# Kernel optimization log

Hardware: AMD Instinct MI355X
Metric: run time of the kernel (lower is better)

The kernel has to match this reference:

```python
import jax, jax.numpy as jnp
import numpy as np

N_NODES = 2048
N_EDGES = 8192
EDGE_DIM = 10
EDGE_HIDDEN = 32
HID = 160


def nnconv(x, edge_index, edge_attr, w1, b1, w2, b2, root, bias):
    """PyG-style NNConv with aggr='mean'.
    x: [N, HID], edge_attr: [E, EDGE_DIM], edge_index: [2, E] (src, dst).
    Per-edge weight W_e = MLP(e) reshaped to [HID, HID]; message = x[src] @ W_e,
    mean-aggregated at dst, plus root transform and bias.
    """
    n = x.shape[0]
    h = jax.nn.relu(edge_attr @ w1 + b1)                     # [E, EDGE_HIDDEN]
    W = (h @ w2 + b2).reshape(-1, HID, HID)                  # [E, HID, HID]
    src, dst = edge_index[0], edge_index[1]
    msg = jnp.einsum('ei,eio->eo', x[src], W)                # [E, HID]
    summed = jax.ops.segment_sum(msg, dst, num_segments=n)   # [N, HID]
    cnt = jax.ops.segment_sum(jnp.ones((msg.shape[0],), x.dtype), dst,
                              num_segments=n)
    aggr = summed / jnp.maximum(cnt, 1.0)[:, None]           # mean; 0 for isolated
    return aggr + x @ root + bias


def setup_inputs() -> dict:
    key = jax.random.key(0)
    ks = jax.random.split(key, 16)
    s = 1.0 / np.sqrt(HID)
    se = 1.0 / np.sqrt(EDGE_DIM)
    sh = 1.0 / np.sqrt(EDGE_HIDDEN)
    inp = {
        'x': jax.random.normal(ks[0], (N_NODES, HID), jnp.float32),
        'edge_attr': jax.random.uniform(ks[1], (N_EDGES, EDGE_DIM), jnp.float32),
        # conv1 (subgraph_conv1) params
        'w1_a': jax.random.normal(ks[2], (EDGE_DIM, EDGE_HIDDEN), jnp.float32) * se,
        'b1_a': jnp.zeros((EDGE_HIDDEN,), jnp.float32),
        'w2_a': jax.random.normal(ks[3], (EDGE_HIDDEN, HID * HID), jnp.float32) * sh,
        'b2_a': jnp.zeros((HID * HID,), jnp.float32),
        'root_a': jax.random.normal(ks[4], (HID, HID), jnp.float32) * s,
        'bias_a': jnp.zeros((HID,), jnp.float32),
        # conv2 (subgraph_conv2, applied twice) params
        'w1_b': jax.random.normal(ks[5], (EDGE_DIM, EDGE_HIDDEN), jnp.float32) * se,
        'b1_b': jnp.zeros((EDGE_HIDDEN,), jnp.float32),
        'w2_b': jax.random.normal(ks[6], (EDGE_HIDDEN, HID * HID), jnp.float32) * sh,
        'b2_b': jnp.zeros((HID * HID,), jnp.float32),
        'root_b': jax.random.normal(ks[7], (HID, HID), jnp.float32) * s,
        'bias_b': jnp.zeros((HID,), jnp.float32),
        'edge_index': jax.random.randint(ks[8], (2, N_EDGES), 0, N_NODES, jnp.int64),
    }
    return inp


def reference(x, edge_attr, w1_a, b1_a, w2_a, b2_a, root_a, bias_a,
              w1_b, b1_b, w2_b, b2_b, root_b, bias_b, edge_index):
    # subgraph_conv1 -> ReLU -> subgraph_conv2 -> ReLU -> subgraph_conv2
    h = jax.nn.relu(nnconv(x, edge_index, edge_attr,
                           w1_a, b1_a, w2_a, b2_a, root_a, bias_a))
    h = jax.nn.relu(nnconv(h, edge_index, edge_attr,
                           w1_b, b1_b, w2_b, b2_b, root_b, bias_b))
    h = nnconv(h, edge_index, edge_attr,
               w1_b, b1_b, w2_b, b2_b, root_b, bias_b)
    return h
```

## Files before the change

kernel.cpp:

```cpp
#include <hip/hip_runtime.h>

#define NN 2048
#define NE 8192
#define ED 10
#define EH 32
#define HID 160
#define NCOL 5504

typedef __attribute__((ext_vector_type(8))) short short8;
typedef __attribute__((ext_vector_type(4))) float f32x4;
typedef unsigned int u32;

__device__ __forceinline__ ushort f2bf(float v) {
    u32 u = __float_as_uint(v);
    u += 0x7FFF + ((u >> 16) & 1);
    return (ushort)(u >> 16);
}
__device__ __forceinline__ float bf2f(ushort u) {
    return __uint_as_float(((u32)u) << 16);
}
__device__ __forceinline__ void gl2lds16(const ushort* g, ushort* l) {
    __builtin_amdgcn_global_load_lds(
        (const __attribute__((address_space(1))) u32*)g,
        (__attribute__((address_space(3))) u32*)l, 16, 0, 0);
}

__global__ __launch_bounds__(256) void k_prep(
        const float* __restrict__ x, ushort* __restrict__ xb,
        const float* __restrict__ ea,
        const float* __restrict__ w1a, const float* __restrict__ b1a,
        const float* __restrict__ w1b, const float* __restrict__ b1b,
        float* __restrict__ ha, float* __restrict__ hb,
        const float* __restrict__ w2a, const float* __restrict__ b2a,
        const float* __restrict__ roota,
        const float* __restrict__ w2b, const float* __restrict__ b2b,
        const float* __restrict__ rootb,
        ushort* __restrict__ BtA, ushort* __restrict__ BtB,
        const int* __restrict__ ei, int* __restrict__ doff,
        int* __restrict__ degg, float* __restrict__ dinv,
        int* __restrict__ delist) {
    __shared__ char smem[20608];
    int b = blockIdx.x, t = threadIdx.x;

    if (b < 512) {
        int set = b >> 8, rel = b & 255;
        const float* w1 = set ? w1b : w1a;
        const float* b1 = set ? b1b : b1a;
        float* h = set ? hb : ha;
        int idx = rel * 1024 + t * 4;
        int e = idx >> 5, j0 = idx & 31;
        float o4[4];
#pragma unroll
        for (int u = 0; u < 4; ++u) {
            float acc = b1[j0 + u];
#pragma unroll
            for (int i = 0; i < ED; ++i) acc += ea[e * ED + i] * w1[i * EH + j0 + u];
            o4[u] = fmaxf(acc, 0.f);
        }
        *(float4*)&h[idx] = *(const float4*)o4;
        return;
    }
    if (b < 856) {
        int rel = b - 512;
        int set = rel / 172, pb = rel - set * 172;
        float (*tile)[161] = (float(*)[161])smem;
        const float* w2 = set ? w2b : w2a;
        const float* b2 = set ? b2b : b2a;
        const float* root = set ? rootb : roota;
        ushort* Bt = set ? BtB : BtA;
        const float* src;
        int n0, zero = 0;
        if (pb < 160)      { int q = pb / 5, op = pb - q * 5; n0 = q * 160 + op * 32; src = w2 + q * 25600 + op * 32; }
        else if (pb < 165) { int ip = pb - 160; n0 = 5120 + ip * 32; src = b2 + ip * 32; }
        else if (pb < 170) { int ip = pb - 165; n0 = 5280 + ip * 32; src = root + ip * 32; }
        else               { n0 = 5440 + (pb - 170) * 32; src = b2; zero = 1; }
        int kl = t >> 5, ol = t & 31;
#pragma unroll
        for (int pass = 0; pass < 20; ++pass) {
            int k = pass * 8 + kl;
            tile[ol][k] = zero ? 0.f : src[k * HID + ol];
        }
        __syncthreads();
        int on = t >> 3, j = t & 7;
        int n = n0 + on;
#pragma unroll
        for (int i = 0; i < 20; i += 2) {
            int k = j * 20 + i;
            u32 pk = ((u32)f2bf(tile[on][k + 1]) << 16) | f2bf(tile[on][k]);
            *(u32*)&Bt[(size_t)n * HID + k] = pk;
        }
        return;
    }
    if (b < 1176) {
        int idx = (b - 856) * 1024 + t * 4;
        float4 xv = *(const float4*)&x[idx];
        ushort o4[4] = {f2bf(xv.x), f2bf(xv.y), f2bf(xv.z), f2bf(xv.w)};
        *(u32*)&xb[idx] = *(const u32*)&o4[0];
        *(u32*)&xb[idx + 2] = *(const u32*)&o4[2];
        return;
    }
    int* deg = (int*)smem;
    int* cur = deg + NN;
    int* part = cur + NN;
    for (int i = t; i < NN; i += 256) deg[i] = 0;
    __syncthreads();
    for (int e = t; e < NE; e += 256) atomicAdd(&deg[ei[NE + e]], 1);
    __syncthreads();
    int loc[8], s = 0;
#pragma unroll
    for (int i = 0; i < 8; ++i) { loc[i] = s; s += deg[t * 8 + i]; }
    part[t] = s;
    __syncthreads();
    int tot = s;
    for (int st = 1; st < 256; st <<= 1) {
        int v = (t >= st) ? part[t - st] : 0;
        __syncthreads();
        part[t] += v;
        __syncthreads();
    }
    int base = part[t] - tot;
#pragma unroll
    for (int i = 0; i < 8; ++i) {
        int d = t * 8 + i;
        doff[d] = base + loc[i];
        cur[d] = base + loc[i];
        degg[d] = deg[d];
        dinv[d] = 1.0f / fmaxf((float)deg[d], 1.0f);
    }
    __syncthreads();
    for (int e = t; e < NE; e += 256) {
        int d = ei[NE + e];
        int p = atomicAdd(&cur[d], 1);
        delist[p] = e;
    }
}

__global__ __launch_bounds__(256) void k_gemm(const ushort* __restrict__ A,
                                              const ushort* __restrict__ B,
                                              ushort* __restrict__ G) {
    __shared__ ushort sA[128 * 32], sB[128 * 32];
    int tid = threadIdx.x;
    int bn = blockIdx.x * 128, bm = blockIdx.y * 128;
    int wid = tid >> 6, lane = tid & 63;
    int wm = (wid >> 1) * 64, wn = (wid & 1) * 64;
    int lr = lane & 15, lk = lane >> 4;
    f32x4 acc[4][4];
#pragma unroll
    for (int i = 0; i < 4; ++i)
#pragma unroll
        for (int j = 0; j < 4; ++j) acc[i][j] = (f32x4){0.f, 0.f, 0.f, 0.f};

    for (int c = 0; c < 5; ++c) {
        int k0 = c * 32;
#pragma unroll
        for (int i = 0; i < 2; ++i) {
            int s = tid + i * 256;
            int r = s >> 2, go = (s & 3) * 8;
            gl2lds16(&A[(size_t)(bm + r) * HID + k0 + go], &sA[s * 8]);
            gl2lds16(&B[(size_t)(bn + r) * HID + k0 + go], &sB[s * 8]);
        }
        __syncthreads();
        short8 av[4];
#pragma unroll
        for (int mt = 0; mt < 4; ++mt)
            av[mt] = *(const short8*)&sA[(wm + mt * 16 + lr) * 32 + lk * 8];
#pragma unroll
        for (int nt = 0; nt < 4; ++nt) {
            short8 bv = *(const short8*)&sB[(wn + nt * 16 + lr) * 32 + lk * 8];
#pragma unroll
            for (int mt = 0; mt < 4; ++mt)
                acc[mt][nt] = __builtin_amdgcn_mfma_f32_16x16x32_bf16(av[mt], bv, acc[mt][nt], 0, 0, 0);
        }
        __syncthreads();
    }
#pragma unroll
    for (int mt = 0; mt < 4; ++mt)
#pragma unroll
        for (int nt = 0; nt < 4; ++nt) {
            int m0 = bm + wm + mt * 16 + lk * 4;
            int n = bn + wn + nt * 16 + lr;
#pragma unroll
            for (int r = 0; r < 4; ++r)
                G[(size_t)(m0 + r) * NCOL + n] = f2bf(acc[mt][nt][r]);
        }
}

__global__ __launch_bounds__(160) void k_aggr(const ushort* __restrict__ G,
        const float* __restrict__ h, const int* __restrict__ ei,
        const int* __restrict__ doff, const int* __restrict__ degg,
        const float* __restrict__ dinv, const int* __restrict__ delist,
        const float* __restrict__ bias, ushort* __restrict__ xn,
        float* __restrict__ out, int last) {
    __shared__ float hbuf[16 * EH];
    __shared__ int ebuf[16], sbuf[16];
    int d = blockIdx.x, t = threadIdx.x;
    int o0 = doff[d], dg = degg[d];
    float acc = 0.f;
    for (int c0 = 0; c0 < dg; c0 += 16) {
        int nc = min(16, dg - c0);
        if (t < nc) {
            int e = delist[o0 + c0 + t];
            ebuf[t] = e;
            sbuf[t] = ei[e];
        }
        __syncthreads();
        for (int i = t; i < nc * EH; i += 160)
            hbuf[i] = h[ebuf[i >> 5] * EH + (i & 31)];
        __syncthreads();
        for (int j = 0; j < nc; ++j) {
            const ushort* Gr = G + (size_t)sbuf[j] * NCOL;
            const float* hj = &hbuf[j * EH];
            float a = bf2f(Gr[5120 + t]);
#pragma unroll
            for (int q = 0; q < 32; ++q)
                a += hj[q] * bf2f(Gr[q * HID + t]);
            acc += a;
        }
        __syncthreads();
    }
    float v = acc * dinv[d] + bf2f(G[(size_t)d * NCOL + 5280 + t]) + bias[t];
    if (last) out[d * HID + t] = v;
    else      xn[d * HID + t] = f2bf(fmaxf(v, 0.f));
}

extern "C" void kernel_launch(void* const* d_in, const int* in_sizes, int n_in,
                              void* d_out, int out_size, void* d_ws, size_t ws_size,
                              hipStream_t stream) {
    const float* x     = (const float*)d_in[0];
    const float* ea    = (const float*)d_in[1];
    const float* w1a   = (const float*)d_in[2];
    const float* b1a   = (const float*)d_in[3];
    const float* w2a   = (const float*)d_in[4];
    const float* b2a   = (const float*)d_in[5];
    const float* roota = (const float*)d_in[6];
    const float* biasa = (const float*)d_in[7];
    const float* w1b   = (const float*)d_in[8];
    const float* b1b   = (const float*)d_in[9];
    const float* w2b   = (const float*)d_in[10];
    const float* b2b   = (const float*)d_in[11];
    const float* rootb = (const float*)d_in[12];
    const float* biasb = (const float*)d_in[13];
    const int*   ei    = (const int*)d_in[14];
    float* out = (float*)d_out;

    char* p = (char*)d_ws;
    ushort* G = (ushort*)p;    p += (size_t)NN * NCOL * 2;
    ushort* BtA = (ushort*)p;  p += (size_t)NCOL * HID * 2;
    ushort* BtB = (ushort*)p;  p += (size_t)NCOL * HID * 2;
    float* h_a = (float*)p;    p += (size_t)NE * EH * 4;
    float* h_b = (float*)p;    p += (size_t)NE * EH * 4;
    ushort* xb0 = (ushort*)p;  p += (size_t)NN * HID * 2;
    ushort* xn = (ushort*)p;   p += (size_t)NN * HID * 2;
    int* doff = (int*)p;       p += NN * 4;
    int* degg = (int*)p;       p += NN * 4;
    float* dinv = (float*)p;   p += NN * 4;
    int* delist = (int*)p;     p += NE * 4;

    k_prep<<<1177, 256, 0, stream>>>(x, xb0, ea, w1a, b1a, w1b, b1b, h_a, h_b,
                                     w2a, b2a, roota, w2b, b2b, rootb, BtA, BtB,
                                     ei, doff, degg, dinv, delist);

    struct Layer { const ushort *xin, *bt; const float *h, *bias; int last; };
    Layer L[3] = {
        {xb0, BtA, h_a, biasa, 0},
        {xn,  BtB, h_b, biasb, 0},
        {xn,  BtB, h_b, biasb, 1},
    };
    for (int l = 0; l < 3; ++l) {
        k_gemm<<<dim3(NCOL / 128, NN / 128), 256, 0, stream>>>(L[l].xin, L[l].bt, G);
        k_aggr<<<NN, 160, 0, stream>>>(G, L[l].h, ei, doff, degg, dinv, delist,
                                       L[l].bias, xn, out, L[l].last);
    }
}
```

Before: 196.8 us.

## Overlap prep work with first GEMM and vectorize aggregation across input rows

The prep kernel is split in two. Only the x conversion and conv1 weight transpose stay ahead of the first GEMM; the edge MLP, conv2 weight transpose and CSR build run as extra blocks inside the first GEMM launch. The aggregation kernel is reworked so each thread handles 8 output columns for a group of 4 hidden rows using 16-byte bf16 loads, followed by a shared-memory reduction across the 8 row groups. The weight-transpose tile now stores bf16 instead of float to shrink LDS use. The intent is to hide prep latency behind the GEMM and cut scalar global loads in the gather, at the cost of an extra reduction pass and mixed block types within one launch.

```diff
diff --git a/kernel.cpp b/kernel.cpp
--- a/kernel.cpp
+++ b/kernel.cpp
@@ -25,80 +25,133 @@
         (__attribute__((address_space(3))) u32*)l, 16, 0, 0);
 }
 
-__global__ __launch_bounds__(256) void k_prep(
+__device__ __forceinline__ void bt_panel(int pb, const float* w2, const float* b2,
+                                         const float* root, ushort* Bt,
+                                         char* smem, int t) {
+    ushort (*tile)[168] = (ushort(*)[168])smem;
+    const float* src;
+    int n0, zero = 0;
+    if (pb < 160)      { int q = pb / 5, op = pb - q * 5; n0 = q * 160 + op * 32; src = w2 + q * 25600 + op * 32; }
+    else if (pb < 165) { int ip = pb - 160; n0 = 5120 + ip * 32; src = b2 + ip * 32; }
+    else if (pb < 170) { int ip = pb - 165; n0 = 5280 + ip * 32; src = root + ip * 32; }
+    else               { n0 = 5440 + (pb - 170) * 32; src = b2; zero = 1; }
+    int kl = t >> 5, ol = t & 31;
+#pragma unroll
+    for (int pass = 0; pass < 20; ++pass) {
+        int k = pass * 8 + kl;
+        tile[ol][k] = zero ? (ushort)0 : f2bf(src[k * HID + ol]);
+    }
+    __syncthreads();
+    int on = t >> 3, j = t & 7;
+    int n = n0 + on;
+#pragma unroll
+    for (int i = 0; i < 20; i += 2) {
+        int k = j * 20 + i;
+        u32 pk = ((u32)tile[on][k + 1] << 16) | tile[on][k];
+        *(u32*)&Bt[(size_t)n * HID + k] = pk;
+    }
+}
+
+__device__ __forceinline__ void gemm_tile(int task, const ushort* A,
+                                          const ushort* Bt, ushort* G,
+                                          char* smem, int t) {
+    ushort* sA = (ushort*)smem;
+    ushort* sB = (ushort*)(smem + 8192);
+    int bn = (task % 43) * 128, bm = (task / 43) * 128;
+    int wid = t >> 6, lane = t & 63;
+    int wm = (wid >> 1) * 64, wn = (wid & 1) * 64;
+    int lr = lane & 15, lk = lane >> 4;
+    f32x4 acc[4][4];
+#pragma unroll
+    for (int i = 0; i < 4; ++i)
+#pragma unroll
+        for (int j = 0; j < 4; ++j) acc[i][j] = (f32x4){0.f, 0.f, 0.f, 0.f};
+    for (int c = 0; c < 5; ++c) {
+        int k0 = c * 32;
+#pragma unroll
+        for (int i = 0; i < 2; ++i) {
+            int s = t + i * 256;
+            int r = s >> 2, go = (s & 3) * 8;
+            gl2lds16(&A[(size_t)(bm + r) * HID + k0 + go], &sA[s * 8]);
+            gl2lds16(&Bt[(size_t)(bn + r) * HID + k0 + go], &sB[s * 8]);
+        }
+        __syncthreads();
+        short8 av[4];
+#pragma unroll
+        for (int mt = 0; mt < 4; ++mt)
+            av[mt] = *(const short8*)&sA[(wm + mt * 16 + lr) * 32 + lk * 8];
+#pragma unroll
+        for (int nt = 0; nt < 4; ++nt) {
+            short8 bv = *(const short8*)&sB[(wn + nt * 16 + lr) * 32 + lk * 8];
+#pragma unroll
+            for (int mt = 0; mt < 4; ++mt)
+                acc[mt][nt] = __builtin_amdgcn_mfma_f32_16x16x32_bf16(av[mt], bv, acc[mt][nt], 0, 0, 0);
+        }
+        __syncthreads();
+    }
+#pragma unroll
+    for (int mt = 0; mt < 4; ++mt)
+#pragma unroll
+        for (int nt = 0; nt < 4; ++nt) {
+            int m0 = bm + wm + mt * 16 + lk * 4;
+            int n = bn + wn + nt * 16 + lr;
+#pragma unroll
+            for (int r = 0; r < 4; ++r)
+                G[(size_t)(m0 + r) * NCOL + n] = f2bf(acc[mt][nt][r]);
+        }
+}
+
+__global__ __launch_bounds__(256) void k_prep1(
         const float* __restrict__ x, ushort* __restrict__ xb,
-        const float* __restrict__ ea,
-        const float* __restrict__ w1a, const float* __restrict__ b1a,
-        const float* __restrict__ w1b, const float* __restrict__ b1b,
-        float* __restrict__ ha, float* __restrict__ hb,
         const float* __restrict__ w2a, const float* __restrict__ b2a,
-        const float* __restrict__ roota,
-        const float* __restrict__ w2b, const float* __restrict__ b2b,
-        const float* __restrict__ rootb,
-        ushort* __restrict__ BtA, ushort* __restrict__ BtB,
-        const int* __restrict__ ei, int* __restrict__ doff,
-        int* __restrict__ degg, float* __restrict__ dinv,
-        int* __restrict__ delist) {
-    __shared__ char smem[20608];
+        const float* __restrict__ roota, ushort* __restrict__ BtA) {
+    __shared__ char smem[10752];
     int b = blockIdx.x, t = threadIdx.x;
-
-    if (b < 512) {
-        int set = b >> 8, rel = b & 255;
-        const float* w1 = set ? w1b : w1a;
-        const float* b1 = set ? b1b : b1a;
-        float* h = set ? hb : ha;
-        int idx = rel * 1024 + t * 4;
-        int e = idx >> 5, j0 = idx & 31;
-        float o4[4];
-#pragma unroll
-        for (int u = 0; u < 4; ++u) {
-            float acc = b1[j0 + u];
-#pragma unroll
-            for (int i = 0; i < ED; ++i) acc += ea[e * ED + i] * w1[i * EH + j0 + u];
-            o4[u] = fmaxf(acc, 0.f);
-        }
-        *(float4*)&h[idx] = *(const float4*)o4;
-        return;
-    }
-    if (b < 856) {
-        int rel = b - 512;
-        int set = rel / 172, pb = rel - set * 172;
-        float (*tile)[161] = (float(*)[161])smem;
-        const float* w2 = set ? w2b : w2a;
-        const float* b2 = set ? b2b : b2a;
-        const float* root = set ? rootb : roota;
-        ushort* Bt = set ? BtB : BtA;
-        const float* src;
-        int n0, zero = 0;
-        if (pb < 160)      { int q = pb / 5, op = pb - q * 5; n0 = q * 160 + op * 32; src = w2 + q * 25600 + op * 32; }
-        else if (pb < 165) { int ip = pb - 160; n0 = 5120 + ip * 32; src = b2 + ip * 32; }
-        else if (pb < 170) { int ip = pb - 165; n0 = 5280 + ip * 32; src = root + ip * 32; }
-        else               { n0 = 5440 + (pb - 170) * 32; src = b2; zero = 1; }
-        int kl = t >> 5, ol = t & 31;
-#pragma unroll
-        for (int pass = 0; pass < 20; ++pass) {
-            int k = pass * 8 + kl;
-            tile[ol][k] = zero ? 0.f : src[k * HID + ol];
-        }
-        __syncthreads();
-        int on = t >> 3, j = t & 7;
-        int n = n0 + on;
-#pragma unroll
-        for (int i = 0; i < 20; i += 2) {
-            int k = j * 20 + i;
-            u32 pk = ((u32)f2bf(tile[on][k + 1]) << 16) | f2bf(tile[on][k]);
-            *(u32*)&Bt[(size_t)n * HID + k] = pk;
-        }
-        return;
-    }
-    if (b < 1176) {
-        int idx = (b - 856) * 1024 + t * 4;
+    if (b < 320) {
+        int idx = b * 1024 + t * 4;
         float4 xv = *(const float4*)&x[idx];
         ushort o4[4] = {f2bf(xv.x), f2bf(xv.y), f2bf(xv.z), f2bf(xv.w)};
         *(u32*)&xb[idx] = *(const u32*)&o4[0];
         *(u32*)&xb[idx + 2] = *(const u32*)&o4[2];
         return;
     }
+    bt_panel(b - 320, w2a, b2a, roota, BtA, smem, t);
+}
+
+__global__ __launch_bounds__(256) void k_gemmP(
+        const ushort* __restrict__ A, const ushort* __restrict__ Bt,
+        ushort* __restrict__ G, const float* __restrict__ ea,
+        const float* __restrict__ w1a, const float* __restrict__ b1a,
+        const float* __restrict__ w1b, const float* __restrict__ b1b,
+        float* __restrict__ ha, float* __restrict__ hb,
+        const float* __restrict__ w2b, const float* __restrict__ b2b,
+        const float* __restrict__ rootb, ushort* __restrict__ BtB,
+        const int* __restrict__ ei, int* __restrict__ doff,
+        int* __restrict__ degg, float* __restrict__ dinv,
+        int* __restrict__ delist) {
+    __shared__ char smem[17408];
+    int b = blockIdx.x, t = threadIdx.x;
+    if (b < 688) { gemm_tile(b, A, Bt, G, smem, t); return; }
+    if (b < 1200) {
+        int rel = b - 688;
+        int set = rel >> 8;
+        const float* w1 = set ? w1b : w1a;
+        const float* b1 = set ? b1b : b1a;
+        float* h = set ? hb : ha;
+        int idx = (rel & 255) * 1024 + t * 4;
+        int e = idx >> 5, j0 = idx & 31;
+        float o4[4];
+#pragma unroll
+        for (int u = 0; u < 4; ++u) {
+            float acc = b1[j0 + u];
+#pragma unroll
+            for (int i = 0; i < ED; ++i) acc += ea[e * ED + i] * w1[i * EH + j0 + u];
+            o4[u] = fmaxf(acc, 0.f);
+        }
+        *(float4*)&h[idx] = *(const float4*)o4;
+        return;
+    }
+    if (b < 1372) { bt_panel(b - 1200, w2b, b2b, rootb, BtB, smem, t); return; }
     int* deg = (int*)smem;
     int* cur = deg + NN;
     int* part = cur + NN;
@@ -130,59 +183,16 @@
     __syncthreads();
     for (int e = t; e < NE; e += 256) {
         int d = ei[NE + e];
-        int p = atomicAdd(&cur[d], 1);
-        delist[p] = e;
+        int pp = atomicAdd(&cur[d], 1);
+        delist[pp] = e;
     }
 }
 
 __global__ __launch_bounds__(256) void k_gemm(const ushort* __restrict__ A,
-                                              const ushort* __restrict__ B,
+                                              const ushort* __restrict__ Bt,
                                               ushort* __restrict__ G) {
-    __shared__ ushort sA[128 * 32], sB[128 * 32];
-    int tid = threadIdx.x;
-    int bn = blockIdx.x * 128, bm = blockIdx.y * 128;
-    int wid = tid >> 6, lane = tid & 63;
-    int wm = (wid >> 1) * 64, wn = (wid & 1) * 64;
-    int lr = lane & 15, lk = lane >> 4;
-    f32x4 acc[4][4];
-#pragma unroll
-    for (int i = 0; i < 4; ++i)
-#pragma unroll
-        for (int j = 0; j < 4; ++j) acc[i][j] = (f32x4){0.f, 0.f, 0.f, 0.f};
-
-    for (int c = 0; c < 5; ++c) {
-        int k0 = c * 32;
-#pragma unroll
-        for (int i = 0; i < 2; ++i) {
-            int s = tid + i * 256;
-            int r = s >> 2, go = (s & 3) * 8;
-            gl2lds16(&A[(size_t)(bm + r) * HID + k0 + go], &sA[s * 8]);
-            gl2lds16(&B[(size_t)(bn + r) * HID + k0 + go], &sB[s * 8]);
-        }
-        __syncthreads();
-        short8 av[4];
-#pragma unroll
-        for (int mt = 0; mt < 4; ++mt)
-            av[mt] = *(const short8*)&sA[(wm + mt * 16 + lr) * 32 + lk * 8];
-#pragma unroll
-        for (int nt = 0; nt < 4; ++nt) {
-            short8 bv = *(const short8*)&sB[(wn + nt * 16 + lr) * 32 + lk * 8];
-#pragma unroll
-            for (int mt = 0; mt < 4; ++mt)
-                acc[mt][nt] = __builtin_amdgcn_mfma_f32_16x16x32_bf16(av[mt], bv, acc[mt][nt], 0, 0, 0);
-        }
-        __syncthreads();
-    }
-#pragma unroll
-    for (int mt = 0; mt < 4; ++mt)
-#pragma unroll
-        for (int nt = 0; nt < 4; ++nt) {
-            int m0 = bm + wm + mt * 16 + lk * 4;
-            int n = bn + wn + nt * 16 + lr;
-#pragma unroll
-            for (int r = 0; r < 4; ++r)
-                G[(size_t)(m0 + r) * NCOL + n] = f2bf(acc[mt][nt][r]);
-        }
+    __shared__ char smem[16384];
+    gemm_tile(blockIdx.x, A, Bt, G, smem, threadIdx.x);
 }
 
 __global__ __launch_bounds__(160) void k_aggr(const ushort* __restrict__ G,
@@ -193,9 +203,14 @@
         float* __restrict__ out, int last) {
     __shared__ float hbuf[16 * EH];
     __shared__ int ebuf[16], sbuf[16];
+    __shared__ float red[8][168];
     int d = blockIdx.x, t = threadIdx.x;
+    int og = t % 20, qg = t / 20;
+    int o8 = og * 8;
     int o0 = doff[d], dg = degg[d];
-    float acc = 0.f;
+    float acc[8];
+#pragma unroll
+    for (int r = 0; r < 8; ++r) acc[r] = 0.f;
     for (int c0 = 0; c0 < dg; c0 += 16) {
         int nc = min(16, dg - c0);
         if (t < nc) {
@@ -209,18 +224,33 @@
         __syncthreads();
         for (int j = 0; j < nc; ++j) {
             const ushort* Gr = G + (size_t)sbuf[j] * NCOL;
-            const float* hj = &hbuf[j * EH];
-            float a = bf2f(Gr[5120 + t]);
-#pragma unroll
-            for (int q = 0; q < 32; ++q)
-                a += hj[q] * bf2f(Gr[q * HID + t]);
-            acc += a;
-        }
-        __syncthreads();
-    }
-    float v = acc * dinv[d] + bf2f(G[(size_t)d * NCOL + 5280 + t]) + bias[t];
-    if (last) out[d * HID + t] = v;
-    else      xn[d * HID + t] = f2bf(fmaxf(v, 0.f));
+            float4 hq = *(const float4*)&hbuf[j * EH + qg * 4];
+            short8 v0 = *(const short8*)&Gr[(qg * 4 + 0) * HID + o8];
+            short8 v1 = *(const short8*)&Gr[(qg * 4 + 1) * HID + o8];
+            short8 v2 = *(const short8*)&Gr[(qg * 4 + 2) * HID + o8];
+            short8 v3 = *(const short8*)&Gr[(qg * 4 + 3) * HID + o8];
+#pragma unroll
+            for (int r = 0; r < 8; ++r)
+                acc[r] += hq.x * bf2f((ushort)v0[r]) + hq.y * bf2f((ushort)v1[r])
+                        + hq.z * bf2f((ushort)v2[r]) + hq.w * bf2f((ushort)v3[r]);
+            if (qg == 0) {
+                short8 vb = *(const short8*)&Gr[5120 + o8];
+#pragma unroll
+                for (int r = 0; r < 8; ++r) acc[r] += bf2f((ushort)vb[r]);
+            }
+        }
+        __syncthreads();
+    }
+#pragma unroll
+    for (int r = 0; r < 8; ++r) red[qg][o8 + r] = acc[r];
+    __syncthreads();
+    if (t < HID) {
+        float s = red[0][t] + red[1][t] + red[2][t] + red[3][t]
+                + red[4][t] + red[5][t] + red[6][t] + red[7][t];
+        float v = s * dinv[d] + bf2f(G[(size_t)d * NCOL + 5280 + t]) + bias[t];
+        if (last) out[d * HID + t] = v;
+        else      xn[d * HID + t] = f2bf(fmaxf(v, 0.f));
+    }
 }
 
 extern "C" void kernel_launch(void* const* d_in, const int* in_sizes, int n_in,
@@ -256,19 +286,16 @@
     float* dinv = (float*)p;   p += NN * 4;
     int* delist = (int*)p;     p += NE * 4;
 
-    k_prep<<<1177, 256, 0, stream>>>(x, xb0, ea, w1a, b1a, w1b, b1b, h_a, h_b,
-                                     w2a, b2a, roota, w2b, b2b, rootb, BtA, BtB,
-                                     ei, doff, degg, dinv, delist);
-
-    struct Layer { const ushort *xin, *bt; const float *h, *bias; int last; };
-    Layer L[3] = {
-        {xb0, BtA, h_a, biasa, 0},
-        {xn,  BtB, h_b, biasb, 0},
-        {xn,  BtB, h_b, biasb, 1},
-    };
-    for (int l = 0; l < 3; ++l) {
-        k_gemm<<<dim3(NCOL / 128, NN / 128), 256, 0, stream>>>(L[l].xin, L[l].bt, G);
-        k_aggr<<<NN, 160, 0, stream>>>(G, L[l].h, ei, doff, degg, dinv, delist,
-                                       L[l].bias, xn, out, L[l].last);
-    }
-}
+    k_prep1<<<492, 256, 0, stream>>>(x, xb0, w2a, b2a, roota, BtA);
+    k_gemmP<<<1373, 256, 0, stream>>>(xb0, BtA, G, ea, w1a, b1a, w1b, b1b,
+                                      h_a, h_b, w2b, b2b, rootb, BtB,
+                                      ei, doff, degg, dinv, delist);
+    k_aggr<<<NN, 160, 0, stream>>>(G, h_a, ei, doff, degg, dinv, delist,
+                                   biasa, xn, out, 0);
+    k_gemm<<<688, 256, 0, stream>>>(xn, BtB, G);
+    k_aggr<<<NN, 160, 0, stream>>>(G, h_b, ei, doff, degg, dinv, delist,
+                                   biasb, xn, out, 0);
+    k_gemm<<<688, 256, 0, stream>>>(xn, BtB, G);
+    k_aggr<<<NN, 160, 0, stream>>>(G, h_b, ei, doff, degg, dinv, delist,
+                                   biasb, xn, out, 1);
+}
```

New measurement: 201.7 us. 1.03x slower.
